# Performance work log

Measured on AMD Instinct MI355X. Metric: run time of the kernel, lower is better.

## Reference

```python
import jax, jax.numpy as jnp
import numpy as np

N = 50000
E = 800000
IN_C = 128
HID = 32
HEADS = 4
G = 512      # number of graphs in batch
OUT_C = 100
NEG_SLOPE = 0.2
EPS = 1e-16


def _gat_params(key, f_in, heads, c):
    k1, k2, k3, k4 = jax.random.split(key, 4)
    s = 1.0 / np.sqrt(f_in)
    return {
        'W': jax.random.uniform(k1, (heads * c, f_in), jnp.float32, -s, s),
        'att_src': jax.random.normal(k2, (heads, c), jnp.float32) * 0.1,
        'att_dst': jax.random.normal(k3, (heads, c), jnp.float32) * 0.1,
        'b': jnp.zeros((heads * c,), jnp.float32),
    }


def setup_inputs() -> dict:
    key = jax.random.key(0)
    ks = jax.random.split(key, 8)
    x = jax.random.normal(ks[0], (N, IN_C), jnp.float32)
    edge_index = jax.random.randint(ks[1], (2, E), 0, N, jnp.int64)
    batch = jnp.sort(jax.random.randint(ks[2], (N,), 0, G, jnp.int64))
    p1 = _gat_params(ks[3], IN_C, HEADS, HID)
    p2 = _gat_params(ks[4], HEADS * HID, HEADS, HID)
    p3 = _gat_params(ks[5], HEADS * HID, HEADS, HID)
    s = 1.0 / np.sqrt(HEADS * HID)
    fc_W = jax.random.uniform(ks[6], (OUT_C, HEADS * HID), jnp.float32, -s, s)
    fc_b = jnp.zeros((OUT_C,), jnp.float32)
    return {
        'x': x, 'edge_index': edge_index, 'batch': batch,
        'W1': p1['W'], 'as1': p1['att_src'], 'ad1': p1['att_dst'], 'b1': p1['b'],
        'W2': p2['W'], 'as2': p2['att_src'], 'ad2': p2['att_dst'], 'b2': p2['b'],
        'W3': p3['W'], 'as3': p3['att_src'], 'ad3': p3['att_dst'], 'b3': p3['b'],
        'fc_W': fc_W, 'fc_b': fc_b,
    }


def gat_conv(x, src, dst, W, att_src, att_dst, b):
    # x: [N, F_in] -> h: [N, H, C]
    h = (x @ W.T).reshape(N, HEADS, HID)
    a_src = jnp.einsum('nhc,hc->nh', h, att_src)   # [N, H]
    a_dst = jnp.einsum('nhc,hc->nh', h, att_dst)
    alpha = a_src[src] + a_dst[dst]                 # [E', H]
    alpha = jax.nn.leaky_relu(alpha, NEG_SLOPE)
    # segment softmax over incoming edges of each dst node
    m = jax.ops.segment_max(alpha, dst, num_segments=N)
    alpha = jnp.exp(alpha - m[dst])
    denom = jax.ops.segment_sum(alpha, dst, num_segments=N)
    alpha = alpha / (denom[dst] + EPS)
    msg = alpha[:, :, None] * h[src]                # [E', H, C]
    out = jax.ops.segment_sum(msg, dst, num_segments=N)
    return out.reshape(N, HEADS * HID) + b


def reference(x, edge_index, batch,
              W1, as1, ad1, b1, W2, as2, ad2, b2, W3, as3, ad3, b3,
              fc_W, fc_b):
    # add self loops (PyG GATConv default)
    loops = jnp.arange(N, dtype=edge_index.dtype)
    src = jnp.concatenate([edge_index[0], loops])
    dst = jnp.concatenate([edge_index[1], loops])
    h = jax.nn.elu(gat_conv(x, src, dst, W1, as1, ad1, b1))
    h = jax.nn.elu(gat_conv(h, src, dst, W2, as2, ad2, b2))
    h = jax.nn.elu(gat_conv(h, src, dst, W3, as3, ad3, b3))
    # global mean pool over graphs
    sums = jax.ops.segment_sum(h, batch, num_segments=G)        # [G, H*C]
    cnts = jax.ops.segment_sum(jnp.ones((N,), h.dtype), batch, num_segments=G)
    pooled = sums / jnp.maximum(cnts, 1.0)[:, None]
    # dropout p=0.5 is identity in eval mode
    return pooled @ fc_W.T + fc_b
```

## Files before the change

### kernel.cpp

```cpp
#include <hip/hip_runtime.h>
#include <math.h>

#define NN 50000
#define EE 800000
#define GG 512
#define OUTC 100
#define NEG 0.2f
#define STRIDE 64
#define NPART 8
#define PRNG (NN / NPART)
#define PCHUNK 4096
#define NCHUNK 196
#define SCAT_BLOCKS (NPART * NCHUNK)

typedef __attribute__((ext_vector_type(8))) short bf16x8;
typedef __attribute__((ext_vector_type(8))) short s16x8;
typedef __attribute__((ext_vector_type(8))) unsigned short us8;
typedef __attribute__((ext_vector_type(4))) float f32x4;

__device__ inline ushort f2bf(float v) {
  unsigned u = __float_as_uint(v);
  unsigned r = (u + 0x7fff + ((u >> 16) & 1)) >> 16;
  return (ushort)r;
}

__global__ __launch_bounds__(256) void k_scatter_prep(const int* __restrict__ ei,
    int* __restrict__ cursor, ushort* __restrict__ srcs,
    const float* __restrict__ W0, const float* __restrict__ W1, const float* __restrict__ W2,
    const float* __restrict__ as0, const float* __restrict__ as1, const float* __restrict__ as2,
    const float* __restrict__ ad0, const float* __restrict__ ad1, const float* __restrict__ ad2,
    ushort* __restrict__ hi, ushort* __restrict__ lo) {
  if (blockIdx.x < SCAT_BLOCKS) {
    int part = blockIdx.x & (NPART - 1);
    int chunk = blockIdx.x >> 3;
    int plo = part * PRNG, phi = plo + PRNG;
    int base = chunk * PCHUNK + (threadIdx.x << 2);
    int4 d[4];
    bool lv[4];
#pragma unroll
    for (int it = 0; it < 4; ++it) {
      int e = base + (it << 10);
      lv[it] = (e < EE);
      if (lv[it]) d[it] = *(const int4*)&ei[EE + e];
      else        d[it] = make_int4(-1, -1, -1, -1);
    }
#pragma unroll
    for (int it = 0; it < 4; ++it) {
      if (!lv[it]) continue;
      int e = base + (it << 10);
      int4 dd = d[it];
      bool m0 = (dd.x >= plo) & (dd.x < phi);
      bool m1 = (dd.y >= plo) & (dd.y < phi);
      bool m2 = (dd.z >= plo) & (dd.z < phi);
      bool m3 = (dd.w >= plo) & (dd.w < phi);
      if (m0 | m1 | m2 | m3) {
        int4 s4 = *(const int4*)&ei[e];
        if (m0) { int p = atomicAdd(&cursor[dd.x], 1); if (p < STRIDE) srcs[(dd.x << 6) + p] = (ushort)s4.x; }
        if (m1) { int p = atomicAdd(&cursor[dd.y], 1); if (p < STRIDE) srcs[(dd.y << 6) + p] = (ushort)s4.y; }
        if (m2) { int p = atomicAdd(&cursor[dd.z], 1); if (p < STRIDE) srcs[(dd.z << 6) + p] = (ushort)s4.z; }
        if (m3) { int p = atomicAdd(&cursor[dd.w], 1); if (p < STRIDE) srcs[(dd.w << 6) + p] = (ushort)s4.w; }
      }
    }
  } else {
    int pb = blockIdx.x - SCAT_BLOCKS;
    int layer = pb / 68, bx = pb % 68;
    const float* W  = (layer == 0) ? W0 : (layer == 1) ? W1 : W2;
    const float* av = (layer == 0) ? as0 : (layer == 1) ? as1 : as2;
    const float* dv = (layer == 0) ? ad0 : (layer == 1) ? ad1 : ad2;
    ushort* hiL = hi + (size_t)layer * 144 * 128;
    ushort* loL = lo + (size_t)layer * 144 * 128;
    int idx = bx * 256 + threadIdx.x;
    if (bx < 64) {
      float v = W[idx];
      ushort hb = f2bf(v);
      float hf = __uint_as_float(((unsigned)hb) << 16);
      hiL[idx] = hb;
      loL[idx] = f2bf(v - hf);
    } else {
      int j2 = idx - 64 * 256;
      int j = j2 >> 7, k = j2 & 127;
      int head = j & 3;
      const float* vec = (j < 4) ? &av[head * 32] : &dv[head * 32];
      float dot = 0.f;
#pragma unroll
      for (int c = 0; c < 32; c++) dot += W[(head * 32 + c) * 128 + k] * vec[c];
      ushort hb = f2bf(dot);
      float hf = __uint_as_float(((unsigned)hb) << 16);
      hiL[(128 + j) * 128 + k] = hb;
      loL[(128 + j) * 128 + k] = f2bf(dot - hf);
      hiL[(136 + j) * 128 + k] = 0;
      loL[(136 + j) * 128 + k] = 0;
    }
  }
}

template <bool TAIL>
__device__ __forceinline__ void gemm_core(const float* __restrict__ feat,
    const ushort* __restrict__ Whi, const ushort* __restrict__ Wlo,
    short* __restrict__ hq, float* __restrict__ asp,
    float* __restrict__ adstf, int n0, int t) {
  int wave = t >> 6, lane = t & 63;
  int quad = lane >> 4, r16 = lane & 15;
  int rowA = n0 + wave * 16 + r16;

  f32x4 acc[9];
#pragma unroll
  for (int nt = 0; nt < 9; nt++) acc[nt] = (f32x4)0.f;

#pragma unroll
  for (int ks = 0; ks < 4; ks++) {
    bf16x8 ah, al;
    {
      float4 va, vb;
      if (TAIL && rowA >= NN) {
        va = make_float4(0.f, 0.f, 0.f, 0.f); vb = va;
      } else {
        const float4* fp = (const float4*)&feat[(size_t)rowA * 128 + ks * 32 + quad * 8];
        va = fp[0]; vb = fp[1];
      }
      float vv[8] = {va.x, va.y, va.z, va.w, vb.x, vb.y, vb.z, vb.w};
      us8 hh, ll;
#pragma unroll
      for (int j = 0; j < 8; j++) {
        ushort hb = f2bf(vv[j]);
        float hf = __uint_as_float(((unsigned)hb) << 16);
        hh[j] = hb;
        ll[j] = (ushort)(__float_as_uint(vv[j] - hf) >> 16);
      }
      ah = (bf16x8)hh;
      al = (bf16x8)ll;
    }
#pragma unroll
    for (int nt = 0; nt < 9; nt++) {
      int wrow = (nt < 8) ? (nt * 16 + r16) : (128 + r16);
      size_t wo = (size_t)wrow * 128 + ks * 32 + quad * 8;
      bf16x8 bh = *(const bf16x8*)&Whi[wo];
      bf16x8 bl = *(const bf16x8*)&Wlo[wo];
      acc[nt] = __builtin_amdgcn_mfma_f32_16x16x32_bf16(ah, bh, acc[nt], 0, 0, 0);
      acc[nt] = __builtin_amdgcn_mfma_f32_16x16x32_bf16(al, bh, acc[nt], 0, 0, 0);
      acc[nt] = __builtin_amdgcn_mfma_f32_16x16x32_bf16(ah, bl, acc[nt], 0, 0, 0);
    }
  }

#pragma unroll
  for (int reg = 0; reg < 4; reg++) {
    float am = 0.f;
#pragma unroll
    for (int nt = 0; nt < 8; nt++) am = fmaxf(am, fabsf(acc[nt][reg]));
#pragma unroll
    for (int off = 1; off < 16; off <<= 1) am = fmaxf(am, __shfl_xor(am, off));
    int node = n0 + wave * 16 + quad * 4 + reg;
    if (!TAIL || node < NN) {
      float amc = fmaxf(am, 1e-20f);
      float rq = 32767.f / amc;
      if (r16 < 4) asp[node * 8 + r16] = acc[8][reg];
      else if (r16 < 8) adstf[node * 4 + r16 - 4] = acc[8][reg];
      else if (r16 == 8) asp[node * 8 + 4] = amc * (1.f / 32767.f);
      short* dq = &hq[(size_t)node * 128 + r16];
#pragma unroll
      for (int nt = 0; nt < 8; nt++)
        dq[nt * 16] = (short)__float2int_rn(acc[nt][reg] * rq);
    }
  }
}

__global__ __launch_bounds__(256) void k_gemm_mfma(const float* __restrict__ feat,
    const ushort* __restrict__ Whi, const ushort* __restrict__ Wlo,
    short* __restrict__ hq, float* __restrict__ asp,
    float* __restrict__ adstf) {
  int n0 = blockIdx.x * 64;
  if (n0 + 64 <= NN)
    gemm_core<false>(feat, Whi, Wlo, hq, asp, adstf, n0, threadIdx.x);
  else
    gemm_core<true>(feat, Whi, Wlo, hq, asp, adstf, n0, threadIdx.x);
}

__global__ __launch_bounds__(256) void k_gather(const short* __restrict__ hq,
    const float* __restrict__ asp,
    const float4* __restrict__ adst,
    const int* __restrict__ cursor, const ushort* __restrict__ srcs,
    const float* __restrict__ bias, float* __restrict__ outf) {
  __shared__ alignas(16) int   s_src[2][4][4][16];
  __shared__ alignas(16) float s_wt[2][4][4][4][20];

  int wave = threadIdx.x >> 6, lane = threadIdx.x & 63;
  int grp = lane >> 4;
  int gl = lane & 15;
  int node = blockIdx.x * 16 + wave * 4 + grp;
  int head = gl >> 2;
  int c0 = gl << 3;

  int deg = 0, e0 = 0;
  float4 ad = make_float4(0.f, 0.f, 0.f, 0.f);
  if (node < NN) {
    deg = min(cursor[node], STRIDE);
    e0 = node << 6;
    ad = adst[node];
  }
  int rounds = (deg + 15) >> 4;

  float acc[8];
#pragma unroll
  for (int i = 0; i < 8; i++) acc[i] = 0.f;
  float ws0 = 0.f, ws1 = 0.f, ws2 = 0.f, ws3 = 0.f;
  float wself = 0.f;

  int nsn = 0, nlive = 0;

  auto phase1 = [&](int r) {
    int j = (r << 4) + gl;
    nlive = (j < deg);
    nsn = nlive ? (int)srcs[e0 + j] : 0;
  };

  auto phase2 = [&](int b) {
    float q0 = 0.f, q1 = 0.f, q2 = 0.f, q3 = 0.f;
    if (nlive) {
      const float4 a = *(const float4*)&asp[nsn * 8];
      float sc = asp[nsn * 8 + 4];
      float v, w0, w1, w2, w3;
      v = a.x + ad.x; v = v > 0.f ? v : NEG * v; w0 = __expf(v);
      v = a.y + ad.y; v = v > 0.f ? v : NEG * v; w1 = __expf(v);
      v = a.z + ad.z; v = v > 0.f ? v : NEG * v; w2 = __expf(v);
      v = a.w + ad.w; v = v > 0.f ? v : NEG * v; w3 = __expf(v);
      ws0 += w0; ws1 += w1; ws2 += w2; ws3 += w3;
      q0 = w0 * sc; q1 = w1 * sc; q2 = w2 * sc; q3 = w3 * sc;
    }
    s_src[b][wave][grp][gl] = nsn << 7;
    s_wt[b][wave][grp][0][gl] = q0;
    s_wt[b][wave][grp][1][gl] = q1;
    s_wt[b][wave][grp][2][gl] = q2;
    s_wt[b][wave][grp][3][gl] = q3;
  };

  auto consume = [&](int r, int b) {
    int cnt = deg - (r << 4);
    cnt = min(cnt, 16);
    const int* srow = &s_src[b][wave][grp][0];
    const float* wrow = &s_wt[b][wave][grp][head][0];
#pragma unroll
    for (int c = 0; c < 2; ++c) {
      int k0 = c << 3;
      if (k0 < cnt) {
        int4 sa = *(const int4*)&srow[k0];
        int4 sb = *(const int4*)&srow[k0 + 4];
        float4 wa = *(const float4*)&wrow[k0];
        float4 wb = *(const float4*)&wrow[k0 + 4];
        s16x8 qa = *(const s16x8*)&hq[sa.x + c0];
        s16x8 qb = *(const s16x8*)&hq[sa.y + c0];
        s16x8 qc = *(const s16x8*)&hq[sa.z + c0];
        s16x8 qd = *(const s16x8*)&hq[sa.w + c0];
        s16x8 qe = *(const s16x8*)&hq[sb.x + c0];
        s16x8 qf = *(const s16x8*)&hq[sb.y + c0];
        s16x8 qg = *(const s16x8*)&hq[sb.z + c0];
        s16x8 qh = *(const s16x8*)&hq[sb.w + c0];
#pragma unroll
        for (int i = 0; i < 8; i++) acc[i] = fmaf(wa.x, (float)qa[i], acc[i]);
#pragma unroll
        for (int i = 0; i < 8; i++) acc[i] = fmaf(wa.y, (float)qb[i], acc[i]);
#pragma unroll
        for (int i = 0; i < 8; i++) acc[i] = fmaf(wa.z, (float)qc[i], acc[i]);
#pragma unroll
        for (int i = 0; i < 8; i++) acc[i] = fmaf(wa.w, (float)qd[i], acc[i]);
        if (k0 + 4 < cnt) {
#pragma unroll
          for (int i = 0; i < 8; i++) acc[i] = fmaf(wb.x, (float)qe[i], acc[i]);
#pragma unroll
          for (int i = 0; i < 8; i++) acc[i] = fmaf(wb.y, (float)qf[i], acc[i]);
#pragma unroll
          for (int i = 0; i < 8; i++) acc[i] = fmaf(wb.z, (float)qg[i], acc[i]);
#pragma unroll
          for (int i = 0; i < 8; i++) acc[i] = fmaf(wb.w, (float)qh[i], acc[i]);
        }
      }
    }
  };

  phase1(0);

  if (node < NN) {
    const float4 a = *(const float4*)&asp[node * 8];
    float sc = asp[node * 8 + 4];
    float v, w0, w1, w2, w3;
    v = a.x + ad.x; v = v > 0.f ? v : NEG * v; w0 = __expf(v);
    v = a.y + ad.y; v = v > 0.f ? v : NEG * v; w1 = __expf(v);
    v = a.z + ad.z; v = v > 0.f ? v : NEG * v; w2 = __expf(v);
    v = a.w + ad.w; v = v > 0.f ? v : NEG * v; w3 = __expf(v);
    float wh = (head == 0) ? w0 : (head == 1) ? w1 : (head == 2) ? w2 : w3;
    wself = wh;
    float wssc = wh * sc;
    s16x8 qs = *(const s16x8*)&hq[(node << 7) + c0];
#pragma unroll
    for (int i = 0; i < 8; i++) acc[i] = wssc * (float)qs[i];
  }

  if (rounds > 0) {
    phase2(0);
    for (int r = 0; r < rounds; ++r) {
      int b = r & 1;
      if (r + 1 < rounds) phase1(r + 1);
      consume(r, b);
      if (r + 1 < rounds) phase2(b ^ 1);
    }
  }

#pragma unroll
  for (int off = 1; off < 16; off <<= 1) {
    ws0 += __shfl_xor(ws0, off);
    ws1 += __shfl_xor(ws1, off);
    ws2 += __shfl_xor(ws2, off);
    ws3 += __shfl_xor(ws3, off);
  }

  if (node < NN) {
    float wsum = wself + ((head == 0) ? ws0 : (head == 1) ? ws1 : (head == 2) ? ws2 : ws3);
    float rcp = 1.f / (wsum + 1e-16f);
    float4 bv0 = *(const float4*)&bias[c0];
    float4 bv1 = *(const float4*)&bias[c0 + 4];
    float bb[8] = {bv0.x, bv0.y, bv0.z, bv0.w, bv1.x, bv1.y, bv1.z, bv1.w};
    float o[8];
#pragma unroll
    for (int i = 0; i < 8; i++) {
      float v = acc[i] * rcp + bb[i];
      o[i] = v > 0.f ? v : expm1f(v);
    }
    *(float4*)&outf[(size_t)node * 128 + c0] = make_float4(o[0], o[1], o[2], o[3]);
    *(float4*)&outf[(size_t)node * 128 + c0 + 4] = make_float4(o[4], o[5], o[6], o[7]);
  }
}

__global__ __launch_bounds__(128) void k_pool(const float* __restrict__ feat,
    const int* __restrict__ batch, float* __restrict__ pooled, float* __restrict__ cnt) {
  int n0 = blockIdx.x * 32;
  int c = threadIdx.x;
  float acc = 0.f; int curg = -1;
  for (int i = 0; i < 32; i++) {
    int n = n0 + i;
    if (n >= NN) break;
    int g = batch[n];
    if (g != curg) {
      if (curg >= 0) atomicAdd(&pooled[curg * 128 + c], acc);
      acc = 0.f; curg = g;
    }
    acc += feat[n * 128 + c];
  }
  if (curg >= 0) atomicAdd(&pooled[curg * 128 + c], acc);
  if (threadIdx.x == 0) {
    float cc = 0.f; int cg = -1;
    for (int i = 0; i < 32; i++) {
      int n = n0 + i;
      if (n >= NN) break;
      int g = batch[n];
      if (g != cg) { if (cg >= 0) atomicAdd(&cnt[cg], cc); cc = 0.f; cg = g; }
      cc += 1.f;
    }
    if (cg >= 0) atomicAdd(&cnt[cg], cc);
  }
}

__global__ __launch_bounds__(128) void k_fc(const float* __restrict__ pooled,
    const float* __restrict__ cnt, const float* __restrict__ fcW,
    const float* __restrict__ fcb, float* __restrict__ out) {
  int g = blockIdx.x;
  __shared__ float p[128];
  int t = threadIdx.x;
  float inv = 1.0f / fmaxf(cnt[g], 1.0f);
  p[t] = pooled[g * 128 + t] * inv;
  __syncthreads();
  if (t < OUTC) {
    float acc = fcb[t];
    const float4* wr = (const float4*)&fcW[t * 128];
    const float4* pp = (const float4*)p;
#pragma unroll
    for (int i = 0; i < 32; i++) {
      float4 w = wr[i], pv = pp[i];
      acc = fmaf(w.x, pv.x, fmaf(w.y, pv.y, fmaf(w.z, pv.z, fmaf(w.w, pv.w, acc))));
    }
    out[g * OUTC + t] = acc;
  }
}

extern "C" void kernel_launch(void* const* d_in, const int* in_sizes, int n_in,
                              void* d_out, int out_size, void* d_ws, size_t ws_size,
                              hipStream_t stream) {
  const float* x    = (const float*)d_in[0];
  const int*   ei   = (const int*)d_in[1];
  const int*   batch= (const int*)d_in[2];
  const float* W1   = (const float*)d_in[3];
  const float* as1  = (const float*)d_in[4];
  const float* ad1  = (const float*)d_in[5];
  const float* b1   = (const float*)d_in[6];
  const float* W2   = (const float*)d_in[7];
  const float* as2  = (const float*)d_in[8];
  const float* ad2  = (const float*)d_in[9];
  const float* b2   = (const float*)d_in[10];
  const float* W3   = (const float*)d_in[11];
  const float* as3  = (const float*)d_in[12];
  const float* ad3  = (const float*)d_in[13];
  const float* b3   = (const float*)d_in[14];
  const float* fcW  = (const float*)d_in[15];
  const float* fcb  = (const float*)d_in[16];
  float* out = (float*)d_out;

  char* p = (char*)d_ws;
  auto alloc = [&](size_t bytes) { char* r = p; p += (bytes + 255) & ~(size_t)255; return r; };
  short* hq     = (short*)alloc((size_t)NN * 128 * 2);
  float* asp    = (float*)alloc((size_t)NN * 8 * 4);
  float* buf0   = (float*)alloc((size_t)NN * 128 * 4);
  float* adstv  = (float*)alloc((size_t)NN * 4 * 4);
  char*  zbase  = p;
  int*   cursor = (int*)alloc((size_t)NN * 4);
  float* pooled = (float*)alloc((size_t)GG * 128 * 4);
  float* cnt    = (float*)alloc((size_t)GG * 4);
  size_t zlen   = (size_t)(p - zbase);
  ushort* srcs  = (ushort*)alloc((size_t)NN * STRIDE * 2);
  ushort* whi   = (ushort*)alloc((size_t)3 * 144 * 128 * 2);
  ushort* wlo   = (ushort*)alloc((size_t)3 * 144 * 128 * 2);

  hipMemsetAsync(zbase, 0, zlen, stream);

  k_scatter_prep<<<SCAT_BLOCKS + 204, 256, 0, stream>>>(ei, cursor, srcs,
      W1, W2, W3, as1, as2, as3, ad1, ad2, ad3, whi, wlo);

  const float* bs[3] = {b1, b2, b3};
  const float* fin = x;
  for (int l = 0; l < 3; l++) {
    k_gemm_mfma<<<(NN + 63) / 64, 256, 0, stream>>>(fin,
        whi + (size_t)l * 144 * 128, wlo + (size_t)l * 144 * 128,
        hq, asp, adstv);
    k_gather<<<(NN + 15) / 16, 256, 0, stream>>>(hq, asp,
        (const float4*)adstv, cursor, srcs, bs[l], buf0);
    fin = buf0;
  }
  k_pool<<<(NN + 31) / 32, 128, 0, stream>>>(buf0, batch, pooled, cnt);
  k_fc<<<GG, 128, 0, stream>>>(pooled, cnt, fcW, fcb, out);
}
```

Baseline: 395.4 us.

## Stage repacked weights into LDS via async global_load_lds in GEMM kernel

Weights are repacked into a chunked [k-chunk][row][8] layout holding hi and lo bf16 parts, with a padded row count so LDS reads are conflict-free. The GEMM block now has 512 threads covering 128 rows and copies each layer's weights into LDS with global_load_lds. Feature loads are issued while that copy is in flight, so the B-operand reads no longer go to global/L2 per MFMA. The cost is about 73 KB of LDS per block, which limits occupancy, and one extra barrier per block.

```diff
diff --git a/kernel.cpp b/kernel.cpp
--- a/kernel.cpp
+++ b/kernel.cpp
@@ -13,6 +13,14 @@
 #define NCHUNK 196
 #define SCAT_BLOCKS (NPART * NCHUNK)
 
+#define WROWS 145
+#define WCHUNKS 73
+#define WLAYER (WCHUNKS * 512)
+
+typedef unsigned int u32;
+#define GLOBAL_AS __attribute__((address_space(1)))
+#define LDS_AS __attribute__((address_space(3)))
+
 typedef __attribute__((ext_vector_type(8))) short bf16x8;
 typedef __attribute__((ext_vector_type(8))) short s16x8;
 typedef __attribute__((ext_vector_type(8))) unsigned short us8;
@@ -29,7 +37,7 @@
     const float* __restrict__ W0, const float* __restrict__ W1, const float* __restrict__ W2,
     const float* __restrict__ as0, const float* __restrict__ as1, const float* __restrict__ as2,
     const float* __restrict__ ad0, const float* __restrict__ ad1, const float* __restrict__ ad2,
-    ushort* __restrict__ hi, ushort* __restrict__ lo) {
+    ushort* __restrict__ wg) {
   if (blockIdx.x < SCAT_BLOCKS) {
     int part = blockIdx.x & (NPART - 1);
     int chunk = blockIdx.x >> 3;
@@ -67,15 +75,16 @@
     const float* W  = (layer == 0) ? W0 : (layer == 1) ? W1 : W2;
     const float* av = (layer == 0) ? as0 : (layer == 1) ? as1 : as2;
     const float* dv = (layer == 0) ? ad0 : (layer == 1) ? ad1 : ad2;
-    ushort* hiL = hi + (size_t)layer * 144 * 128;
-    ushort* loL = lo + (size_t)layer * 144 * 128;
+    ushort* wgL = wg + (size_t)layer * WLAYER;
     int idx = bx * 256 + threadIdx.x;
     if (bx < 64) {
+      int row = idx >> 7, col = idx & 127;
+      int c = col >> 3, j = col & 7;
       float v = W[idx];
       ushort hb = f2bf(v);
       float hf = __uint_as_float(((unsigned)hb) << 16);
-      hiL[idx] = hb;
-      loL[idx] = f2bf(v - hf);
+      wgL[((size_t)c * WROWS + row) * 8 + j] = hb;
+      wgL[((size_t)(16 + c) * WROWS + row) * 8 + j] = f2bf(v - hf);
     } else {
       int j2 = idx - 64 * 256;
       int j = j2 >> 7, k = j2 & 127;
@@ -86,22 +95,49 @@
       for (int c = 0; c < 32; c++) dot += W[(head * 32 + c) * 128 + k] * vec[c];
       ushort hb = f2bf(dot);
       float hf = __uint_as_float(((unsigned)hb) << 16);
-      hiL[(128 + j) * 128 + k] = hb;
-      loL[(128 + j) * 128 + k] = f2bf(dot - hf);
-      hiL[(136 + j) * 128 + k] = 0;
-      loL[(136 + j) * 128 + k] = 0;
-    }
-  }
-}
-
-template <bool TAIL>
-__device__ __forceinline__ void gemm_core(const float* __restrict__ feat,
-    const ushort* __restrict__ Whi, const ushort* __restrict__ Wlo,
-    short* __restrict__ hq, float* __restrict__ asp,
-    float* __restrict__ adstf, int n0, int t) {
+      int c16 = k >> 3, jj = k & 7;
+      wgL[((size_t)c16 * WROWS + 128 + j) * 8 + jj] = hb;
+      wgL[((size_t)(16 + c16) * WROWS + 128 + j) * 8 + jj] = f2bf(dot - hf);
+      wgL[((size_t)c16 * WROWS + 136 + j) * 8 + jj] = 0;
+      wgL[((size_t)(16 + c16) * WROWS + 136 + j) * 8 + jj] = 0;
+    }
+  }
+}
+
+__global__ __launch_bounds__(512) void k_gemm_mfma(const float* __restrict__ feat,
+    const ushort* __restrict__ wg,
+    short* __restrict__ hq, float* __restrict__ asp, float* __restrict__ adstf) {
+  __shared__ alignas(16) ushort lds[WLAYER];
+  int t = threadIdx.x;
   int wave = t >> 6, lane = t & 63;
   int quad = lane >> 4, r16 = lane & 15;
+
+#pragma unroll
+  for (int i = 0; i < 10; ++i) {
+    int chunk = i * 8 + wave;
+    if (chunk < WCHUNKS) {
+      int off = chunk * 512 + lane * 8;
+      __builtin_amdgcn_global_load_lds((const GLOBAL_AS u32*)&wg[off],
+                                       (LDS_AS u32*)&lds[off], 16, 0, 0);
+    }
+  }
+
+  int n0 = blockIdx.x * 128;
   int rowA = n0 + wave * 16 + r16;
+  bool valid = rowA < NN;
+  float4 f[8];
+#pragma unroll
+  for (int ks = 0; ks < 4; ++ks) {
+    if (valid) {
+      const float4* fp = (const float4*)&feat[(size_t)rowA * 128 + ks * 32 + quad * 8];
+      f[ks * 2] = fp[0];
+      f[ks * 2 + 1] = fp[1];
+    } else {
+      f[ks * 2] = make_float4(0.f, 0.f, 0.f, 0.f);
+      f[ks * 2 + 1] = f[ks * 2];
+    }
+  }
+  __syncthreads();
 
   f32x4 acc[9];
 #pragma unroll
@@ -111,13 +147,7 @@
   for (int ks = 0; ks < 4; ks++) {
     bf16x8 ah, al;
     {
-      float4 va, vb;
-      if (TAIL && rowA >= NN) {
-        va = make_float4(0.f, 0.f, 0.f, 0.f); vb = va;
-      } else {
-        const float4* fp = (const float4*)&feat[(size_t)rowA * 128 + ks * 32 + quad * 8];
-        va = fp[0]; vb = fp[1];
-      }
+      float4 va = f[ks * 2], vb = f[ks * 2 + 1];
       float vv[8] = {va.x, va.y, va.z, va.w, vb.x, vb.y, vb.z, vb.w};
       us8 hh, ll;
 #pragma unroll
@@ -130,12 +160,12 @@
       ah = (bf16x8)hh;
       al = (bf16x8)ll;
     }
+    int cc = ks * 4 + quad;
 #pragma unroll
     for (int nt = 0; nt < 9; nt++) {
       int wrow = (nt < 8) ? (nt * 16 + r16) : (128 + r16);
-      size_t wo = (size_t)wrow * 128 + ks * 32 + quad * 8;
-      bf16x8 bh = *(const bf16x8*)&Whi[wo];
-      bf16x8 bl = *(const bf16x8*)&Wlo[wo];
+      bf16x8 bh = *(const bf16x8*)&lds[((size_t)cc * WROWS + wrow) * 8];
+      bf16x8 bl = *(const bf16x8*)&lds[((size_t)(16 + cc) * WROWS + wrow) * 8];
       acc[nt] = __builtin_amdgcn_mfma_f32_16x16x32_bf16(ah, bh, acc[nt], 0, 0, 0);
       acc[nt] = __builtin_amdgcn_mfma_f32_16x16x32_bf16(al, bh, acc[nt], 0, 0, 0);
       acc[nt] = __builtin_amdgcn_mfma_f32_16x16x32_bf16(ah, bl, acc[nt], 0, 0, 0);
@@ -150,7 +180,7 @@
 #pragma unroll
     for (int off = 1; off < 16; off <<= 1) am = fmaxf(am, __shfl_xor(am, off));
     int node = n0 + wave * 16 + quad * 4 + reg;
-    if (!TAIL || node < NN) {
+    if (node < NN) {
       float amc = fmaxf(am, 1e-20f);
       float rq = 32767.f / amc;
       if (r16 < 4) asp[node * 8 + r16] = acc[8][reg];
@@ -162,17 +192,6 @@
         dq[nt * 16] = (short)__float2int_rn(acc[nt][reg] * rq);
     }
   }
-}
-
-__global__ __launch_bounds__(256) void k_gemm_mfma(const float* __restrict__ feat,
-    const ushort* __restrict__ Whi, const ushort* __restrict__ Wlo,
-    short* __restrict__ hq, float* __restrict__ asp,
-    float* __restrict__ adstf) {
-  int n0 = blockIdx.x * 64;
-  if (n0 + 64 <= NN)
-    gemm_core<false>(feat, Whi, Wlo, hq, asp, adstf, n0, threadIdx.x);
-  else
-    gemm_core<true>(feat, Whi, Wlo, hq, asp, adstf, n0, threadIdx.x);
 }
 
 __global__ __launch_bounds__(256) void k_gather(const short* __restrict__ hq,
@@ -414,20 +433,18 @@
   float* cnt    = (float*)alloc((size_t)GG * 4);
   size_t zlen   = (size_t)(p - zbase);
   ushort* srcs  = (ushort*)alloc((size_t)NN * STRIDE * 2);
-  ushort* whi   = (ushort*)alloc((size_t)3 * 144 * 128 * 2);
-  ushort* wlo   = (ushort*)alloc((size_t)3 * 144 * 128 * 2);
+  ushort* wg    = (ushort*)alloc((size_t)3 * WLAYER * 2);
 
   hipMemsetAsync(zbase, 0, zlen, stream);
 
   k_scatter_prep<<<SCAT_BLOCKS + 204, 256, 0, stream>>>(ei, cursor, srcs,
-      W1, W2, W3, as1, as2, as3, ad1, ad2, ad3, whi, wlo);
+      W1, W2, W3, as1, as2, as3, ad1, ad2, ad3, wg);
 
   const float* bs[3] = {b1, b2, b3};
   const float* fin = x;
   for (int l = 0; l < 3; l++) {
-    k_gemm_mfma<<<(NN + 63) / 64, 256, 0, stream>>>(fin,
-        whi + (size_t)l * 144 * 128, wlo + (size_t)l * 144 * 128,
-        hq, asp, adstv);
+    k_gemm_mfma<<<(NN + 127) / 128, 512, 0, stream>>>(fin,
+        wg + (size_t)l * WLAYER, hq, asp, adstv);
     k_gather<<<(NN + 15) / 16, 256, 0, stream>>>(hq, asp,
         (const float4*)adstv, cursor, srcs, bs[l], buf0);
     fin = buf0;
```

Result: faster. 321.6 us (-18.7%).
